# Kernel optimization log

Measured on AMD Instinct MI355X. Metric: run time of the kernel, lower is better.

The kernel has to match this reference:

```python
import jax, jax.numpy as jnp
import numpy as np

D_MODEL = 1024
NHEAD = 16
D_K = D_MODEL // NHEAD
MAX_REL = 1024


def setup_inputs() -> dict:
    key = jax.random.key(0)
    ks = jax.random.split(key, 6)
    B, S = 4, 2048
    s = 1.0 / np.sqrt(D_MODEL)
    x = jax.random.normal(ks[0], (B, S, D_MODEL), dtype=jnp.float32)
    W_qkv = jax.random.normal(ks[1], (D_MODEL, 3 * D_MODEL), dtype=jnp.float32) * s
    b_qkv = jnp.zeros((3 * D_MODEL,), dtype=jnp.float32)
    W_out = jax.random.normal(ks[2], (D_MODEL, D_MODEL), dtype=jnp.float32) * s
    b_out = jnp.zeros((D_MODEL,), dtype=jnp.float32)
    # torch init is zeros; use small random so bias path is exercised
    rel_bias = jax.random.normal(ks[3], (2 * MAX_REL + 1, NHEAD), dtype=jnp.float32) * 0.02
    return {"x": x, "W_qkv": W_qkv, "b_qkv": b_qkv, "W_out": W_out,
            "b_out": b_out, "rel_bias": rel_bias}


def reference(x, W_qkv, b_qkv, W_out, b_out, rel_bias):
    B, S, D = x.shape
    qkv = x @ W_qkv + b_qkv                      # [B,S,3D]
    qkv = qkv.reshape(B, S, 3, NHEAD, D_K)
    q, k, v = qkv[:, :, 0], qkv[:, :, 1], qkv[:, :, 2]  # [B,S,H,dk]
    # scores: [B,H,S,S]
    scores = jnp.einsum('bihd,bjhd->bhij', q, k) / jnp.sqrt(jnp.float32(D_K))
    idxs = jnp.arange(S)
    rel = jnp.clip(idxs[:, None] - idxs[None, :] + MAX_REL, 0, 2 * MAX_REL)  # [S,S]
    bias = rel_bias[rel]                         # [S,S,H]
    scores = scores + jnp.transpose(bias, (2, 0, 1))[None]  # broadcast over batch
    attn = jax.nn.softmax(scores, axis=-1)       # dropout p=0 (eval)
    out = jnp.einsum('bhij,bjhd->bihd', attn, v).reshape(B, S, D)
    return out @ W_out + b_out
```

## Files before the change

### kernel.cpp

```cpp
#include <hip/hip_runtime.h>

#define S_LEN 2048
#define NHEADS 16
#define DK 64
#define DMODEL 1024
#define QSCALE 0.18033688011f

typedef float f32x4 __attribute__((ext_vector_type(4)));
typedef _Float16 f16x8 __attribute__((ext_vector_type(8)));
typedef _Float16 f16x4 __attribute__((ext_vector_type(4)));
typedef __fp16 h16x2 __attribute__((ext_vector_type(2)));

__device__ __forceinline__ unsigned short f2h_bits(float f) {
  _Float16 h = (_Float16)f;
  unsigned short u; __builtin_memcpy(&u, &h, 2); return u;
}

__device__ __forceinline__ f32x4 mfma16(f16x8 a, f16x8 b, f32x4 c) {
  return __builtin_amdgcn_mfma_f32_16x16x32_f16(a, b, c, 0, 0, 0);
}
__device__ __forceinline__ f16x8 frag_ld(const unsigned short* p) {
  return *(const f16x8*)p;
}

#define GLD_LDS(g, l)                                                          \
  __builtin_amdgcn_global_load_lds(                                            \
      (const __attribute__((address_space(1))) void*)(g),                      \
      (__attribute__((address_space(3))) void*)(l), 16, 0, 0)

__global__ void convert_f32_f16(const float* __restrict__ in,
                                unsigned short* __restrict__ out, int n4) {
  int i = blockIdx.x * blockDim.x + threadIdx.x;
  if (i < n4) {
    f32x4 v = *(const f32x4*)(in + (size_t)i * 4);
    unsigned short o[4];
#pragma unroll
    for (int j = 0; j < 4; j++) o[j] = f2h_bits(v[j]);
    *(uint2*)(out + (size_t)i * 4) = *(const uint2*)o;
  }
}

__global__ void transpose_f32_f16(const float* __restrict__ in,
                                  unsigned short* __restrict__ out, int R, int C) {
  __shared__ unsigned short tile[32][33];
  int bx = blockIdx.x * 32, by = blockIdx.y * 32;
  int tx = threadIdx.x, ty = threadIdx.y;
  for (int i = ty; i < 32; i += 8)
    tile[i][tx] = f2h_bits(in[(size_t)(by + i) * C + bx + tx]);
  __syncthreads();
  for (int i = ty; i < 32; i += 8)
    out[(size_t)(bx + i) * R + by + tx] = tile[tx][i];
}

__launch_bounds__(256)
__global__ void gemm_bt(const unsigned short* __restrict__ A,
                        const unsigned short* __restrict__ Bt,
                        int M, int N, int K, int mode,
                        const float* __restrict__ bias,
                        float* __restrict__ out0,
                        unsigned short* __restrict__ q_o,
                        unsigned short* __restrict__ k_o,
                        unsigned short* __restrict__ v_o) {
  __shared__ __attribute__((aligned(16))) unsigned short As[128 * 32];
  __shared__ __attribute__((aligned(16))) unsigned short Bs[128 * 32];
  const int tid = threadIdx.x;
  const int w = tid >> 6, lane = tid & 63;
  const int wm = w >> 1, wn = w & 1;
  const int col = lane & 15, quad = lane >> 4;
  const int m0 = blockIdx.y * 128, n0 = blockIdx.x * 128;
  const f32x4 fzero = {0.f, 0.f, 0.f, 0.f};
  f32x4 acc[4][4];
#pragma unroll
  for (int i = 0; i < 4; i++)
#pragma unroll
    for (int j = 0; j < 4; j++) acc[i][j] = fzero;

  for (int k0 = 0; k0 < K; k0 += 32) {
    __syncthreads();
#pragma unroll
    for (int it = 0; it < 2; it++) {
      int c = it * 256 + tid;
      GLD_LDS(A + (size_t)(m0 + (c >> 2)) * K + k0 + (c & 3) * 8, &As[c * 8]);
      GLD_LDS(Bt + (size_t)(n0 + (c >> 2)) * K + k0 + (c & 3) * 8, &Bs[c * 8]);
    }
    __syncthreads();
    f16x8 af[4], bfr[4];
#pragma unroll
    for (int mi = 0; mi < 4; mi++)
      af[mi] = frag_ld(&As[(wm * 64 + mi * 16 + col) * 32 + quad * 8]);
#pragma unroll
    for (int ni = 0; ni < 4; ni++)
      bfr[ni] = frag_ld(&Bs[(wn * 64 + ni * 16 + col) * 32 + quad * 8]);
#pragma unroll
    for (int mi = 0; mi < 4; mi++)
#pragma unroll
      for (int ni = 0; ni < 4; ni++)
        acc[mi][ni] = mfma16(af[mi], bfr[ni], acc[mi][ni]);
  }

#pragma unroll
  for (int mi = 0; mi < 4; mi++) {
#pragma unroll
    for (int ni = 0; ni < 4; ni++) {
      int gm_b = m0 + wm * 64 + mi * 16 + quad * 4;
      int gn = n0 + wn * 64 + ni * 16 + col;
      float bv = bias[gn];
      if (mode == 1) {
#pragma unroll
        for (int r = 0; r < 4; r++)
          out0[(size_t)(gm_b + r) * N + gn] = acc[mi][ni][r] + bv;
      } else {
        int b = gm_b >> 11, s0 = gm_b & 2047;
        int t = gn >> 10, hd = gn & 1023;
        int h = hd >> 6, d = hd & 63;
        size_t bh = (size_t)(b * NHEADS + h);
        if (t == 2) {
          int pos0 = (s0 & ~31) | ((s0 & 12) << 1) | ((s0 & 16) >> 2);
          unsigned short o4[4];
#pragma unroll
          for (int r = 0; r < 4; r++) o4[r] = f2h_bits(acc[mi][ni][r] + bv);
          *(uint2*)&v_o[(bh * DK + d) * S_LEN + pos0] = *(const uint2*)o4;
        } else {
          unsigned short* dst = (t == 0) ? q_o : k_o;
          float sc = (t == 0) ? QSCALE : 1.0f;
#pragma unroll
          for (int r = 0; r < 4; r++)
            dst[(bh * S_LEN + s0 + r) * DK + d] = f2h_bits((acc[mi][ni][r] + bv) * sc);
        }
      }
    }
  }
}

__launch_bounds__(256, 3)
__global__ void attn_kernel(const unsigned short* __restrict__ Q,
                            const unsigned short* __restrict__ K,
                            const unsigned short* __restrict__ Vt,
                            const float* __restrict__ rel_bias,
                            unsigned short* __restrict__ ctx) {
  __shared__ __attribute__((aligned(16))) char smem[41472];
  unsigned short* Ks = (unsigned short*)smem;
  unsigned short* Vs = (unsigned short*)(smem + 16384);
  float* brev = (float*)(smem + 32768);
  float* lred = (float*)(smem + 41216);
  float* red  = (float*)smem;

  const int tid = threadIdx.x;
  const int w = tid >> 6, lane = tid & 63;
  const int col = lane & 15, quad = lane >> 4;
  const int c7 = col & 7;
  const int bid = blockIdx.x;
  const int xcd = bid & 7, slot = bid >> 3;
  const int bh = (slot >> 5) * 8 + xcd;
  const int qt = slot & 31;
  const int h = bh & (NHEADS - 1), b = bh >> 4;
  const unsigned short* qp = Q + (size_t)bh * S_LEN * DK;
  const unsigned short* kp = K + (size_t)bh * S_LEN * DK;
  const unsigned short* vp = Vt + (size_t)bh * DK * S_LEN;
  const f32x4 fzero = {0.f, 0.f, 0.f, 0.f};

  const int tbase = 1985 - qt * 64;
#pragma unroll
  for (int it = 0; it < 9; it++) {
    int idx = it * 256 + tid;
    if (idx < 2112) {
      int rel = 3072 - (tbase + idx);
      rel = rel < 0 ? 0 : (rel > 2048 ? 2048 : rel);
      brev[idx] = rel_bias[rel * NHEADS + h] * 1.44269504089f;
    }
  }

  f16x8 qb[4][2];
#pragma unroll
  for (int qs = 0; qs < 4; qs++)
#pragma unroll
    for (int ks = 0; ks < 2; ks++)
      qb[qs][ks] = frag_ld(qp + (size_t)(qt * 64 + qs * 16 + col) * DK + ks * 32 + quad * 8);

  f32x4 o[4][4];
  float rsum[4];
#pragma unroll
  for (int qs = 0; qs < 4; qs++) {
#pragma unroll
    for (int ds = 0; ds < 4; ds++) o[qs][ds] = fzero;
    rsum[qs] = 0.f;
  }

  int kaoff[2][2];
#pragma unroll
  for (int jsub = 0; jsub < 2; jsub++)
#pragma unroll
    for (int ks = 0; ks < 2; ks++)
      kaoff[jsub][ks] = (w * 32 + jsub * 16 + col) * 64 + (((ks * 4 + quad) ^ c7) * 8);
  const int vg = w * 4 + quad;
  const int vboff = col * 128 + (((vg & 8) | ((vg & 7) ^ c7)) * 8);

  const int rK = tid >> 3, gK = (tid & 7) ^ (rK & 7);
  const int dV = tid >> 4, gsV = tid & 15;
  const int gV = (gsV & 8) | ((gsV & 7) ^ (dV & 7));
  const unsigned short* ks0 = kp + rK * DK + gK * 8;
  const unsigned short* vs0 = vp + (size_t)dV * S_LEN + gV * 8;
  unsigned short* kd0 = &Ks[tid * 8];
  unsigned short* vd0 = &Vs[tid * 8];

  const float* bq = brev + (w * 32 + quad * 4 - col + 63);

#define COMPUTE(ka, vb)                                                        \
  _Pragma("unroll")                                                            \
  for (int qs = 0; qs < 4; qs++) {                                             \
    h16x2 pk[4];                                                               \
    _Pragma("unroll")                                                          \
    for (int js = 0; js < 2; js++) {                                           \
      f32x4 bias4;                                                             \
      _Pragma("unroll")                                                        \
      for (int r = 0; r < 4; r++) bias4[r] = bq[(js - qs) * 16 + r];           \
      f32x4 sc = mfma16(ka[js][1], qb[qs][1],                                  \
                        mfma16(ka[js][0], qb[qs][0], bias4));                  \
      float p0 = __builtin_amdgcn_exp2f(sc[0]);                                \
      float p1 = __builtin_amdgcn_exp2f(sc[1]);                                \
      float p2 = __builtin_amdgcn_exp2f(sc[2]);                                \
      float p3 = __builtin_amdgcn_exp2f(sc[3]);                                \
      rsum[qs] += (p0 + p1) + (p2 + p3);                                       \
      pk[js * 2]     = __builtin_amdgcn_cvt_pkrtz(p0, p1);                     \
      pk[js * 2 + 1] = __builtin_amdgcn_cvt_pkrtz(p2, p3);                     \
    }                                                                          \
    f16x8 pa;                                                                  \
    __builtin_memcpy(&pa, pk, 16);                                             \
    _Pragma("unroll")                                                          \
    for (int ds = 0; ds < 4; ds++)                                             \
      o[qs][ds] = mfma16(pa, vb[ds], o[qs][ds]);                               \
  }

  for (int ck = 0; ck < S_LEN / 128; ck++) {
    __syncthreads();
#pragma unroll
    for (int it = 0; it < 4; it++) {
      GLD_LDS(ks0 + it * 32 * DK, kd0 + it * 2048);
      GLD_LDS(vs0 + (size_t)it * 16 * S_LEN, vd0 + it * 2048);
    }
    __syncthreads();
    f16x8 ka[2][2];
#pragma unroll
    for (int jsub = 0; jsub < 2; jsub++)
#pragma unroll
      for (int ks = 0; ks < 2; ks++)
        ka[jsub][ks] = frag_ld(&Ks[kaoff[jsub][ks]]);
    f16x8 vb[4];
#pragma unroll
    for (int ds = 0; ds < 4; ds++)
      vb[ds] = frag_ld(&Vs[vboff + ds * 2048]);
    COMPUTE(ka, vb)
    ks0 += 128 * DK; vs0 += 128; bq += 128;
  }

#pragma unroll
  for (int qs = 0; qs < 4; qs++) {
    rsum[qs] += __shfl_xor(rsum[qs], 16);
    rsum[qs] += __shfl_xor(rsum[qs], 32);
  }

  __syncthreads();
  for (int ws = 3; ws >= 0; ws--) {
    if (w == ws) {
#pragma unroll
      for (int qs = 0; qs < 4; qs++) {
#pragma unroll
        for (int ds = 0; ds < 4; ds++) {
#pragma unroll
          for (int r = 0; r < 4; r++) {
            int q = qs * 16 + quad * 4 + r, d = ds * 16 + col;
            if (ws == 3) red[q * 68 + d] = o[qs][ds][r];
            else         red[q * 68 + d] += o[qs][ds][r];
          }
        }
        int ql = qs * 16 + col;
        if (ws == 3) lred[ql] = rsum[qs];
        else         lred[ql] += rsum[qs];
      }
    }
    __syncthreads();
  }

#pragma unroll
  for (int pass = 0; pass < 4; pass++) {
    int ql = w * 16 + pass * 4 + quad;
    f32x4 ov = *(const f32x4*)&red[ql * 68 + col * 4];
    float inv = 1.0f / lred[ql];
    h16x2 lo = __builtin_amdgcn_cvt_pkrtz(ov[0] * inv, ov[1] * inv);
    h16x2 hi = __builtin_amdgcn_cvt_pkrtz(ov[2] * inv, ov[3] * inv);
    uint2 pkd;
    __builtin_memcpy(&pkd.x, &lo, 4);
    __builtin_memcpy(&pkd.y, &hi, 4);
    *(uint2*)&ctx[((size_t)b * S_LEN + qt * 64 + ql) * DMODEL + h * DK + col * 4] = pkd;
  }
}

extern "C" void kernel_launch(void* const* d_in, const int* in_sizes, int n_in,
                              void* d_out, int out_size, void* d_ws, size_t ws_size,
                              hipStream_t stream) {
  (void)in_sizes; (void)n_in; (void)out_size; (void)ws_size;
  const float* x        = (const float*)d_in[0];
  const float* W_qkv    = (const float*)d_in[1];
  const float* b_qkv    = (const float*)d_in[2];
  const float* W_out    = (const float*)d_in[3];
  const float* b_out    = (const float*)d_in[4];
  const float* rel_bias = (const float*)d_in[5];
  float* out = (float*)d_out;

  char* ws = (char*)d_ws;
  unsigned short* xh     = (unsigned short*)(ws + 0);
  unsigned short* ctxh   = (unsigned short*)(ws + 0);
  unsigned short* Wqkv_t = (unsigned short*)(ws + 16777216);
  unsigned short* Wout_t = (unsigned short*)(ws + 23068672);
  unsigned short* Qb     = (unsigned short*)(ws + 25165824);
  unsigned short* Kb     = (unsigned short*)(ws + 41943040);
  unsigned short* Vtb    = (unsigned short*)(ws + 58720256);

  convert_f32_f16<<<(8192 * 1024 / 4 + 255) / 256, 256, 0, stream>>>(x, xh, 8192 * 1024 / 4);
  transpose_f32_f16<<<dim3(3072 / 32, 1024 / 32), dim3(32, 8), 0, stream>>>(W_qkv, Wqkv_t, 1024, 3072);
  transpose_f32_f16<<<dim3(1024 / 32, 1024 / 32), dim3(32, 8), 0, stream>>>(W_out, Wout_t, 1024, 1024);
  gemm_bt<<<dim3(3072 / 128, 8192 / 128), 256, 0, stream>>>(
      xh, Wqkv_t, 8192, 3072, 1024, 0, b_qkv, nullptr, Qb, Kb, Vtb);
  attn_kernel<<<4 * NHEADS * (S_LEN / 64), 256, 0, stream>>>(Qb, Kb, Vtb, rel_bias, ctxh);
  gemm_bt<<<dim3(1024 / 128, 8192 / 128), 256, 0, stream>>>(
      ctxh, Wout_t, 8192, 1024, 1024, 1, b_out, out, nullptr, nullptr, nullptr);
}
```

Baseline: 319.7 us.

## Double-buffer K/V tiles in attention and swizzle GEMM block order across XCDs

The attention kernel now keeps two LDS buffers for K/V chunks and issues global-to-LDS loads for the next chunk before computing on the current one. Explicit vmcnt waits and raw s_barrier calls replace the paired __syncthreads, so memory latency can overlap with MFMA work. LDS use grows to about 74 KB and the launch bound drops from 3 to 2 blocks per CU, which lowers occupancy. Separately, the GEMM remaps block IDs so consecutive tiles land on the same XCD, aiming at better L2 reuse.

```diff
diff --git a/kernel.cpp b/kernel.cpp
--- a/kernel.cpp
+++ b/kernel.cpp
@@ -27,6 +27,11 @@
   __builtin_amdgcn_global_load_lds(                                            \
       (const __attribute__((address_space(1))) void*)(g),                      \
       (__attribute__((address_space(3))) void*)(l), 16, 0, 0)
+
+#define SBAR()  asm volatile("s_barrier" ::: "memory")
+#define WAITV8  asm volatile("s_waitcnt vmcnt(8)" ::: "memory")
+#define WAITV0  asm volatile("s_waitcnt vmcnt(0)" ::: "memory")
+#define WAITL0  asm volatile("s_waitcnt lgkmcnt(0)" ::: "memory")
 
 __global__ void convert_f32_f16(const float* __restrict__ in,
                                 unsigned short* __restrict__ out, int n4) {
@@ -67,7 +72,12 @@
   const int w = tid >> 6, lane = tid & 63;
   const int wm = w >> 1, wn = w & 1;
   const int col = lane & 15, quad = lane >> 4;
-  const int m0 = blockIdx.y * 128, n0 = blockIdx.x * 128;
+  const int nx = gridDim.x;
+  const int nwg = nx * gridDim.y;
+  const int bidl = blockIdx.y * nx + blockIdx.x;
+  const int cpx = nwg >> 3;
+  const int swz = (bidl & 7) * cpx + (bidl >> 3);
+  const int m0 = (swz / nx) * 128, n0 = (swz % nx) * 128;
   const f32x4 fzero = {0.f, 0.f, 0.f, 0.f};
   f32x4 acc[4][4];
 #pragma unroll
@@ -132,17 +142,19 @@
   }
 }
 
-__launch_bounds__(256, 3)
+__launch_bounds__(256, 2)
 __global__ void attn_kernel(const unsigned short* __restrict__ Q,
                             const unsigned short* __restrict__ K,
                             const unsigned short* __restrict__ Vt,
                             const float* __restrict__ rel_bias,
                             unsigned short* __restrict__ ctx) {
-  __shared__ __attribute__((aligned(16))) char smem[41472];
-  unsigned short* Ks = (unsigned short*)smem;
-  unsigned short* Vs = (unsigned short*)(smem + 16384);
-  float* brev = (float*)(smem + 32768);
-  float* lred = (float*)(smem + 41216);
+  __shared__ __attribute__((aligned(16))) char smem[74240];
+  unsigned short* KsA = (unsigned short*)smem;
+  unsigned short* VsA = (unsigned short*)(smem + 16384);
+  unsigned short* KsB = (unsigned short*)(smem + 32768);
+  unsigned short* VsB = (unsigned short*)(smem + 49152);
+  float* brev = (float*)(smem + 65536);
+  float* lred = (float*)(smem + 73984);
   float* red  = (float*)smem;
 
   const int tid = threadIdx.x;
@@ -200,10 +212,20 @@
   const int gV = (gsV & 8) | ((gsV & 7) ^ (dV & 7));
   const unsigned short* ks0 = kp + rK * DK + gK * 8;
   const unsigned short* vs0 = vp + (size_t)dV * S_LEN + gV * 8;
-  unsigned short* kd0 = &Ks[tid * 8];
-  unsigned short* vd0 = &Vs[tid * 8];
+  unsigned short* kdA = &KsA[tid * 8];
+  unsigned short* vdA = &VsA[tid * 8];
+  unsigned short* kdB = &KsB[tid * 8];
+  unsigned short* vdB = &VsB[tid * 8];
 
   const float* bq = brev + (w * 32 + quad * 4 - col + 63);
+
+#define ISSUE8(kd, vd)                                                         \
+  _Pragma("unroll")                                                            \
+  for (int it = 0; it < 4; it++) {                                             \
+    GLD_LDS(ks0 + it * 32 * DK, kd + it * 2048);                               \
+    GLD_LDS(vs0 + (size_t)it * 16 * S_LEN, vd + it * 2048);                    \
+  }                                                                            \
+  ks0 += 128 * DK; vs0 += 128;
 
 #define COMPUTE(ka, vb)                                                        \
   _Pragma("unroll")                                                            \
@@ -231,26 +253,42 @@
       o[qs][ds] = mfma16(pa, vb[ds], o[qs][ds]);                               \
   }
 
-  for (int ck = 0; ck < S_LEN / 128; ck++) {
-    __syncthreads();
-#pragma unroll
-    for (int it = 0; it < 4; it++) {
-      GLD_LDS(ks0 + it * 32 * DK, kd0 + it * 2048);
-      GLD_LDS(vs0 + (size_t)it * 16 * S_LEN, vd0 + it * 2048);
-    }
-    __syncthreads();
-    f16x8 ka[2][2];
-#pragma unroll
-    for (int jsub = 0; jsub < 2; jsub++)
-#pragma unroll
-      for (int ks = 0; ks < 2; ks++)
-        ka[jsub][ks] = frag_ld(&Ks[kaoff[jsub][ks]]);
-    f16x8 vb[4];
-#pragma unroll
-    for (int ds = 0; ds < 4; ds++)
-      vb[ds] = frag_ld(&Vs[vboff + ds * 2048]);
-    COMPUTE(ka, vb)
-    ks0 += 128 * DK; vs0 += 128; bq += 128;
+#define PHASE(Ksb, Vsb)                                                        \
+  {                                                                            \
+    f16x8 ka[2][2];                                                            \
+    _Pragma("unroll")                                                          \
+    for (int jsub = 0; jsub < 2; jsub++)                                       \
+      _Pragma("unroll")                                                        \
+      for (int ks = 0; ks < 2; ks++)                                           \
+        ka[jsub][ks] = frag_ld(&Ksb[kaoff[jsub][ks]]);                         \
+    f16x8 vb[4];                                                               \
+    _Pragma("unroll")                                                          \
+    for (int ds = 0; ds < 4; ds++)                                             \
+      vb[ds] = frag_ld(&Vsb[vboff + ds * 2048]);                               \
+    COMPUTE(ka, vb)                                                            \
+    bq += 128;                                                                 \
+  }
+
+  ISSUE8(kdA, vdA)
+  __syncthreads();
+
+  for (int ck = 0; ck < 16; ck += 2) {
+    ISSUE8(kdB, vdB)
+    WAITV8;
+    SBAR();
+    PHASE(KsA, VsA)
+    WAITL0;
+    SBAR();
+    if (ck < 14) {
+      ISSUE8(kdA, vdA)
+      WAITV8;
+    } else {
+      WAITV0;
+    }
+    SBAR();
+    PHASE(KsB, VsB)
+    WAITL0;
+    SBAR();
   }
 
 #pragma unroll
```

New measurement: 315.3 us. No clear change (-1.4%).
